# Optimization experiments

Measured on AMD Instinct MI355X. Metric: run time of the kernel, lower is better.

## Reference

```python
import jax, jax.numpy as jnp
import numpy as np

H, W = 2048, 4096
NUM_FRAMES, NUM_CAMERAS = 200, 4


def setup_inputs() -> dict:
    key = jax.random.key(0)
    k0, k1, k2, k3, k4 = jax.random.split(key, 5)
    exposure_params = 0.1 * jax.random.normal(k0, (NUM_FRAMES,), dtype=jnp.float32)
    vignetting_params = 0.05 * jax.random.normal(k1, (NUM_CAMERAS, 3, 5), dtype=jnp.float32)
    color_params = 0.05 * jax.random.normal(k2, (NUM_FRAMES, 8), dtype=jnp.float32)
    crf_params = 0.1 * jax.random.normal(k3, (NUM_CAMERAS, 3, 4), dtype=jnp.float32)
    rgb_in = jax.random.uniform(k4, (H, W, 3), dtype=jnp.float32)
    xs = jnp.arange(W, dtype=jnp.float32) + 0.5  # pixel-center x
    ys = jnp.arange(H, dtype=jnp.float32) + 0.5  # pixel-center y
    gx, gy = jnp.meshgrid(xs, ys)  # each [H, W]
    pixel_coords = jnp.stack([gx, gy], axis=-1)  # [H, W, 2] (x, y)
    return {
        'exposure_params': exposure_params,
        'vignetting_params': vignetting_params,
        'color_params': color_params,
        'crf_params': crf_params,
        'rgb_in': rgb_in,
        'pixel_coords': pixel_coords,
        'resolution_w': W,
        'resolution_h': H,
        'camera_idx': 1,
        'frame_idx': 3,
    }


def _ppisp_forward(exposure_params, vignetting_params, color_params, crf_params,
                   rgb_flat, coords_flat, resolution_w, resolution_h,
                   camera_idx, frame_idx):
    # rgb_flat: [N, 3], coords_flat: [N, 2]
    rgb = rgb_flat
    # --- stage 1: per-frame exposure scale ---
    if frame_idx >= 0:
        rgb = rgb * jnp.exp(exposure_params[frame_idx])
    # --- stage 2: per-camera radial vignetting polynomial (per channel) ---
    if camera_idx >= 0:
        vp = vignetting_params[camera_idx]  # [3, 5] = (cx, cy, a1, a2, a3) per channel
        cx = (0.5 + vp[:, 0]) * resolution_w   # [3] optical center x in pixels
        cy = (0.5 + vp[:, 1]) * resolution_h   # [3]
        norm2 = (0.5 * resolution_w) ** 2 + (0.5 * resolution_h) ** 2
        dx = coords_flat[:, :1] - cx           # [N, 3]
        dy = coords_flat[:, 1:] - cy           # [N, 3]
        r2 = (dx * dx + dy * dy) / norm2       # normalized squared radius
        vig = 1.0 + r2 * (vp[:, 2] + r2 * (vp[:, 3] + r2 * vp[:, 4]))  # Horner cubic in r^2
        rgb = rgb * vig
    # --- stage 3: per-frame 8-param color correction (identity-anchored 3x3) ---
    if frame_idx >= 0:
        p = color_params[frame_idx]  # [8]
        one = jnp.ones((), dtype=p.dtype)
        M = jnp.stack([
            jnp.stack([one + p[0], p[1], p[2]]),
            jnp.stack([p[3], one + p[4], p[5]]),
            jnp.stack([p[6], p[7], one]),
        ])  # [3, 3]
        rgb = rgb @ M.T
    # --- stage 4: per-camera CRF gamma curve (per channel, 4 params) ---
    if camera_idx >= 0:
        q = crf_params[camera_idx]      # [3, 4] = (log_gamma, b1, b2, b3)
        gamma = jnp.exp(q[:, 0])        # [3]
        x = jnp.clip(rgb, 0.0, 1.0)
        y = x ** gamma
        # smooth perturbation anchored at y=0 and y=1
        y = y + y * (1.0 - y) * (q[:, 1] + q[:, 2] * y + q[:, 3] * (1.0 - y))
        rgb = y
    return rgb


def reference(exposure_params, vignetting_params, color_params, crf_params,
              rgb_in, pixel_coords, resolution_w, resolution_h, camera_idx, frame_idx):
    original_shape = rgb_in.shape
    rgb_flat = rgb_in.reshape(-1, 3).astype(jnp.float32)
    coords_flat = pixel_coords.reshape(-1, 2).astype(jnp.float32)
    out = _ppisp_forward(exposure_params.astype(jnp.float32),
                         vignetting_params.astype(jnp.float32),
                         color_params.astype(jnp.float32),
                         crf_params.astype(jnp.float32),
                         rgb_flat, coords_flat,
                         int(resolution_w), int(resolution_h),
                         int(camera_idx), int(frame_idx))
    return out.reshape(original_shape)
```

## Files before the change

### kernel.cpp

```cpp
#include <hip/hip_runtime.h>
#include <math.h>

constexpr int W = 4096;
constexpr int H = 2048;
constexpr int W_SHIFT = 12;
constexpr int NPIX = W * H;
constexpr int NFLOAT = NPIX * 3;
constexpr int BLOCK = 256;
constexpr int WAVES = BLOCK / 64;
constexpr int PIX_PER_LANE = 4;
constexpr int FLT_PER_LANE = 3 * PIX_PER_LANE;
constexpr int CHUNK_FLT = 64 * FLT_PER_LANE;
constexpr int CHUNK_PIX = CHUNK_FLT / 3;
constexpr int GRID = NPIX / (WAVES * CHUNK_PIX);

#define AS1 __attribute__((address_space(1)))
#define AS3 __attribute__((address_space(3)))

__global__ __launch_bounds__(BLOCK) void ppisp_kernel(
    const float* __restrict__ exposure,
    const float* __restrict__ vigp,
    const float* __restrict__ colorp,
    const float* __restrict__ crfp,
    const float* __restrict__ rgb_in,
    const int*   __restrict__ cam_idx,
    const int*   __restrict__ frm_idx,
    float*       __restrict__ out)
{
    __shared__ float smem[WAVES][CHUNK_FLT];

    const int t    = threadIdx.x;
    const int wave = t >> 6;
    const int lane = t & 63;

    const int chunk = blockIdx.x * WAVES + wave;
    const size_t f0 = (size_t)chunk * CHUNK_FLT;

    #pragma unroll
    for (int j = 0; j < 3; ++j) {
        __builtin_amdgcn_global_load_lds(
            (const AS1 void*)(rgb_in + f0 + j * 256 + lane * 4),
            (AS3 void*)&smem[wave][j * 256], 16, 0, 0);
    }

    const int cam = cam_idx[0];
    const int frm = frm_idx[0];

    const float escale = (frm >= 0) ? __expf(exposure[frm]) : 1.0f;

    float cx[3], cy[3], a1[3], a2[3], a3[3];
    if (cam >= 0) {
        const float* vp = vigp + cam * 15;
        #pragma unroll
        for (int c = 0; c < 3; ++c) {
            cx[c] = (0.5f + vp[c * 5 + 0]) * (float)W;
            cy[c] = (0.5f + vp[c * 5 + 1]) * (float)H;
            a1[c] = vp[c * 5 + 2];
            a2[c] = vp[c * 5 + 3];
            a3[c] = vp[c * 5 + 4];
        }
    } else {
        #pragma unroll
        for (int c = 0; c < 3; ++c) {
            cx[c] = cy[c] = 0.0f;
            a1[c] = a2[c] = a3[c] = 0.0f;
        }
    }
    const float nx = 0.5f * (float)W, ny = 0.5f * (float)H;
    const float inv_norm2 = 1.0f / (nx * nx + ny * ny);

    float M[9];
    if (frm >= 0) {
        const float* p = colorp + frm * 8;
        M[0] = 1.0f + p[0]; M[1] = p[1];        M[2] = p[2];
        M[3] = p[3];        M[4] = 1.0f + p[4]; M[5] = p[5];
        M[6] = p[6];        M[7] = p[7];        M[8] = 1.0f;
    } else {
        M[0] = 1.0f; M[1] = 0.0f; M[2] = 0.0f;
        M[3] = 0.0f; M[4] = 1.0f; M[5] = 0.0f;
        M[6] = 0.0f; M[7] = 0.0f; M[8] = 1.0f;
    }

    float gam[3], b1[3], b2[3], b3[3];
    const int crf_on = (cam >= 0);
    if (crf_on) {
        const float* q = crfp + cam * 12;
        #pragma unroll
        for (int c = 0; c < 3; ++c) {
            gam[c] = __expf(q[c * 4 + 0]);
            b1[c]  = q[c * 4 + 1];
            b2[c]  = q[c * 4 + 2];
            b3[c]  = q[c * 4 + 3];
        }
    } else {
        #pragma unroll
        for (int c = 0; c < 3; ++c) { gam[c] = 1.0f; b1[c] = b2[c] = b3[c] = 0.0f; }
    }

    asm volatile("s_waitcnt vmcnt(0)" ::: "memory");
    __builtin_amdgcn_sched_barrier(0);

    const float4* sb = (const float4*)smem[wave];
    const float4 x0 = sb[lane * 3 + 0];
    const float4 x1 = sb[lane * 3 + 1];
    const float4 x2 = sb[lane * 3 + 2];

    float v[FLT_PER_LANE];
    v[0] = x0.x; v[1]  = x0.y; v[2]  = x0.z; v[3]  = x0.w;
    v[4] = x1.x; v[5]  = x1.y; v[6]  = x1.z; v[7]  = x1.w;
    v[8] = x2.x; v[9]  = x2.y; v[10] = x2.z; v[11] = x2.w;

    const int pb = chunk * CHUNK_PIX + lane * PIX_PER_LANE;
    #pragma unroll
    for (int k = 0; k < PIX_PER_LANE; ++k) {
        const int p = pb + k;
        const float px = (float)(p & (W - 1)) + 0.5f;
        const float py = (float)(p >> W_SHIFT) + 0.5f;

        float ch[3];
        #pragma unroll
        for (int c = 0; c < 3; ++c) ch[c] = v[k * 3 + c] * escale;

        #pragma unroll
        for (int c = 0; c < 3; ++c) {
            const float dx = px - cx[c];
            const float dy = py - cy[c];
            const float r2 = (dx * dx + dy * dy) * inv_norm2;
            ch[c] *= 1.0f + r2 * (a1[c] + r2 * (a2[c] + r2 * a3[c]));
        }

        float o[3];
        o[0] = M[0] * ch[0] + M[1] * ch[1] + M[2] * ch[2];
        o[1] = M[3] * ch[0] + M[4] * ch[1] + M[5] * ch[2];
        o[2] = M[6] * ch[0] + M[7] * ch[1] + M[8] * ch[2];

        if (crf_on) {
            #pragma unroll
            for (int c = 0; c < 3; ++c) {
                const float x = fminf(fmaxf(o[c], 0.0f), 1.0f);
                float y = exp2f(gam[c] * __log2f(x));
                y = y + y * (1.0f - y) * (b1[c] + b2[c] * y + b3[c] * (1.0f - y));
                o[c] = y;
            }
        }

        v[k * 3 + 0] = o[0];
        v[k * 3 + 1] = o[1];
        v[k * 3 + 2] = o[2];
    }

    float4* og = (float4*)(out + f0 + (size_t)lane * FLT_PER_LANE);
    og[0] = make_float4(v[0], v[1], v[2],  v[3]);
    og[1] = make_float4(v[4], v[5], v[6],  v[7]);
    og[2] = make_float4(v[8], v[9], v[10], v[11]);
}

extern "C" void kernel_launch(void* const* d_in, const int* in_sizes, int n_in,
                              void* d_out, int out_size, void* d_ws, size_t ws_size,
                              hipStream_t stream) {
    const float* exposure = (const float*)d_in[0];
    const float* vigp     = (const float*)d_in[1];
    const float* colorp   = (const float*)d_in[2];
    const float* crfp     = (const float*)d_in[3];
    const float* rgb_in   = (const float*)d_in[4];
    const int* cam_idx = (const int*)d_in[8];
    const int* frm_idx = (const int*)d_in[9];
    float* out = (float*)d_out;

    ppisp_kernel<<<dim3(GRID), dim3(BLOCK), 0, stream>>>(
        exposure, vigp, colorp, crfp, rgb_in, cam_idx, frm_idx, out);
}
```

Baseline: 228.2 us.

## Double pixels per lane and stage output through LDS with coalesced nontemporal stores

Each lane now handles 8 pixels in two halves of 4, loading 6 LDS-staged segments per wave and halving the grid. Results are written back into LDS and then stored to global memory in fully coalesced 16-byte-per-lane rows with nontemporal stores, replacing the old strided 48-byte-per-lane float4 writes. This targets write coalescing and cache pollution on a bandwidth-bound streaming kernel. It costs more LDS per block and fewer blocks in flight, which may reduce occupancy and latency hiding.

After: 222.2 us. 1.03x faster.

```diff
diff --git a/kernel.cpp b/kernel.cpp
--- a/kernel.cpp
+++ b/kernel.cpp
@@ -8,14 +8,16 @@
 constexpr int NFLOAT = NPIX * 3;
 constexpr int BLOCK = 256;
 constexpr int WAVES = BLOCK / 64;
-constexpr int PIX_PER_LANE = 4;
+constexpr int PIX_PER_LANE = 8;
 constexpr int FLT_PER_LANE = 3 * PIX_PER_LANE;
 constexpr int CHUNK_FLT = 64 * FLT_PER_LANE;
 constexpr int CHUNK_PIX = CHUNK_FLT / 3;
-constexpr int GRID = NPIX / (WAVES * CHUNK_PIX);
+constexpr int GRID = NFLOAT / (WAVES * CHUNK_FLT);
 
 #define AS1 __attribute__((address_space(1)))
 #define AS3 __attribute__((address_space(3)))
+
+typedef float floatx4 __attribute__((ext_vector_type(4)));
 
 __global__ __launch_bounds__(BLOCK) void ppisp_kernel(
     const float* __restrict__ exposure,
@@ -37,7 +39,7 @@
     const size_t f0 = (size_t)chunk * CHUNK_FLT;
 
     #pragma unroll
-    for (int j = 0; j < 3; ++j) {
+    for (int j = 0; j < 6; ++j) {
         __builtin_amdgcn_global_load_lds(
             (const AS1 void*)(rgb_in + f0 + j * 256 + lane * 4),
             (AS3 void*)&smem[wave][j * 256], 16, 0, 0);
@@ -100,59 +102,81 @@
     asm volatile("s_waitcnt vmcnt(0)" ::: "memory");
     __builtin_amdgcn_sched_barrier(0);
 
-    const float4* sb = (const float4*)smem[wave];
-    const float4 x0 = sb[lane * 3 + 0];
-    const float4 x1 = sb[lane * 3 + 1];
-    const float4 x2 = sb[lane * 3 + 2];
+    float4* sb = (float4*)smem[wave];
+    float v[FLT_PER_LANE];
+    #pragma unroll
+    for (int h = 0; h < 2; ++h) {
+        #pragma unroll
+        for (int j = 0; j < 3; ++j) {
+            const float4 x = sb[h * 192 + lane * 3 + j];
+            v[h * 12 + 4 * j + 0] = x.x;
+            v[h * 12 + 4 * j + 1] = x.y;
+            v[h * 12 + 4 * j + 2] = x.z;
+            v[h * 12 + 4 * j + 3] = x.w;
+        }
+    }
 
-    float v[FLT_PER_LANE];
-    v[0] = x0.x; v[1]  = x0.y; v[2]  = x0.z; v[3]  = x0.w;
-    v[4] = x1.x; v[5]  = x1.y; v[6]  = x1.z; v[7]  = x1.w;
-    v[8] = x2.x; v[9]  = x2.y; v[10] = x2.z; v[11] = x2.w;
+    #pragma unroll
+    for (int h = 0; h < 2; ++h) {
+        const int pb = chunk * CHUNK_PIX + h * 256 + lane * 4;
+        #pragma unroll
+        for (int k = 0; k < 4; ++k) {
+            const int p = pb + k;
+            const float px = (float)(p & (W - 1)) + 0.5f;
+            const float py = (float)(p >> W_SHIFT) + 0.5f;
 
-    const int pb = chunk * CHUNK_PIX + lane * PIX_PER_LANE;
-    #pragma unroll
-    for (int k = 0; k < PIX_PER_LANE; ++k) {
-        const int p = pb + k;
-        const float px = (float)(p & (W - 1)) + 0.5f;
-        const float py = (float)(p >> W_SHIFT) + 0.5f;
+            float ch[3];
+            #pragma unroll
+            for (int c = 0; c < 3; ++c) ch[c] = v[h * 12 + k * 3 + c] * escale;
 
-        float ch[3];
-        #pragma unroll
-        for (int c = 0; c < 3; ++c) ch[c] = v[k * 3 + c] * escale;
-
-        #pragma unroll
-        for (int c = 0; c < 3; ++c) {
-            const float dx = px - cx[c];
-            const float dy = py - cy[c];
-            const float r2 = (dx * dx + dy * dy) * inv_norm2;
-            ch[c] *= 1.0f + r2 * (a1[c] + r2 * (a2[c] + r2 * a3[c]));
-        }
-
-        float o[3];
-        o[0] = M[0] * ch[0] + M[1] * ch[1] + M[2] * ch[2];
-        o[1] = M[3] * ch[0] + M[4] * ch[1] + M[5] * ch[2];
-        o[2] = M[6] * ch[0] + M[7] * ch[1] + M[8] * ch[2];
-
-        if (crf_on) {
             #pragma unroll
             for (int c = 0; c < 3; ++c) {
-                const float x = fminf(fmaxf(o[c], 0.0f), 1.0f);
-                float y = exp2f(gam[c] * __log2f(x));
-                y = y + y * (1.0f - y) * (b1[c] + b2[c] * y + b3[c] * (1.0f - y));
-                o[c] = y;
+                const float dx = px - cx[c];
+                const float dy = py - cy[c];
+                const float r2 = (dx * dx + dy * dy) * inv_norm2;
+                ch[c] *= 1.0f + r2 * (a1[c] + r2 * (a2[c] + r2 * a3[c]));
             }
+
+            float o[3];
+            o[0] = M[0] * ch[0] + M[1] * ch[1] + M[2] * ch[2];
+            o[1] = M[3] * ch[0] + M[4] * ch[1] + M[5] * ch[2];
+            o[2] = M[6] * ch[0] + M[7] * ch[1] + M[8] * ch[2];
+
+            if (crf_on) {
+                #pragma unroll
+                for (int c = 0; c < 3; ++c) {
+                    const float x = fminf(fmaxf(o[c], 0.0f), 1.0f);
+                    float y = exp2f(gam[c] * __log2f(x));
+                    y = y + y * (1.0f - y) * (b1[c] + b2[c] * y + b3[c] * (1.0f - y));
+                    o[c] = y;
+                }
+            }
+
+            v[h * 12 + k * 3 + 0] = o[0];
+            v[h * 12 + k * 3 + 1] = o[1];
+            v[h * 12 + k * 3 + 2] = o[2];
         }
-
-        v[k * 3 + 0] = o[0];
-        v[k * 3 + 1] = o[1];
-        v[k * 3 + 2] = o[2];
     }
 
-    float4* og = (float4*)(out + f0 + (size_t)lane * FLT_PER_LANE);
-    og[0] = make_float4(v[0], v[1], v[2],  v[3]);
-    og[1] = make_float4(v[4], v[5], v[6],  v[7]);
-    og[2] = make_float4(v[8], v[9], v[10], v[11]);
+    #pragma unroll
+    for (int h = 0; h < 2; ++h) {
+        #pragma unroll
+        for (int j = 0; j < 3; ++j) {
+            sb[h * 192 + lane * 3 + j] =
+                make_float4(v[h * 12 + 4 * j + 0], v[h * 12 + 4 * j + 1],
+                            v[h * 12 + 4 * j + 2], v[h * 12 + 4 * j + 3]);
+        }
+    }
+
+    {
+        const floatx4* sl = (const floatx4*)smem[wave];
+        floatx4* og = (floatx4*)(out + f0);
+        #pragma unroll
+        for (int j = 0; j < 6; ++j) {
+            const floatx4 x = sl[j * 64 + lane];
+            __builtin_nontemporal_store(x, &og[j * 64 + lane]);
+        }
+    }
 }
 
 extern "C" void kernel_launch(void* const* d_in, const int* in_sizes, int n_in,
```

## Convert to persistent grid with 4-deep LDS prefetch pipeline and nontemporal coalesced stores

Applied to the files above, without the earlier changes.

Replaces the one-chunk-per-wave launch with a fixed grid of 768 blocks in which each wave loops over many chunks. Up to three future chunks are kept in flight through global_load_lds into a 4-slot per-wave LDS ring, with explicit vmcnt waits. Results are written back into LDS and then stored to global memory as fully coalesced nontemporal float4 stores instead of strided per-lane stores. This aims to hide load latency and improve write coalescing, but adds LDS traffic and makes correctness depend on hand-set vmcnt counts, and the final iterations clamp their prefetch to reload the last chunk.

After: 228.6 us. No clear change (+0.2%).

```diff
diff --git a/kernel.cpp b/kernel.cpp
--- a/kernel.cpp
+++ b/kernel.cpp
@@ -12,10 +12,16 @@
 constexpr int FLT_PER_LANE = 3 * PIX_PER_LANE;
 constexpr int CHUNK_FLT = 64 * FLT_PER_LANE;
 constexpr int CHUNK_PIX = CHUNK_FLT / 3;
-constexpr int GRID = NPIX / (WAVES * CHUNK_PIX);
+constexpr int NCHUNK = NFLOAT / CHUNK_FLT;
+constexpr int GRID = 768;
+constexpr int NWAVE = GRID * WAVES;
+constexpr int DEPTH = 4;
+constexpr int ITERS = (NCHUNK + NWAVE - 1) / NWAVE;
 
 #define AS1 __attribute__((address_space(1)))
 #define AS3 __attribute__((address_space(3)))
+
+typedef float floatx4 __attribute__((ext_vector_type(4)));
 
 __global__ __launch_bounds__(BLOCK) void ppisp_kernel(
     const float* __restrict__ exposure,
@@ -27,21 +33,12 @@
     const int*   __restrict__ frm_idx,
     float*       __restrict__ out)
 {
-    __shared__ float smem[WAVES][CHUNK_FLT];
+    __shared__ float smem[WAVES][DEPTH][CHUNK_FLT];
 
     const int t    = threadIdx.x;
     const int wave = t >> 6;
     const int lane = t & 63;
-
-    const int chunk = blockIdx.x * WAVES + wave;
-    const size_t f0 = (size_t)chunk * CHUNK_FLT;
-
-    #pragma unroll
-    for (int j = 0; j < 3; ++j) {
-        __builtin_amdgcn_global_load_lds(
-            (const AS1 void*)(rgb_in + f0 + j * 256 + lane * 4),
-            (AS3 void*)&smem[wave][j * 256], 16, 0, 0);
-    }
+    const int wgid = blockIdx.x * WAVES + wave;
 
     const int cam = cam_idx[0];
     const int frm = frm_idx[0];
@@ -98,61 +95,105 @@
     }
 
     asm volatile("s_waitcnt vmcnt(0)" ::: "memory");
-    __builtin_amdgcn_sched_barrier(0);
-
-    const float4* sb = (const float4*)smem[wave];
-    const float4 x0 = sb[lane * 3 + 0];
-    const float4 x1 = sb[lane * 3 + 1];
-    const float4 x2 = sb[lane * 3 + 2];
-
-    float v[FLT_PER_LANE];
-    v[0] = x0.x; v[1]  = x0.y; v[2]  = x0.z; v[3]  = x0.w;
-    v[4] = x1.x; v[5]  = x1.y; v[6]  = x1.z; v[7]  = x1.w;
-    v[8] = x2.x; v[9]  = x2.y; v[10] = x2.z; v[11] = x2.w;
-
-    const int pb = chunk * CHUNK_PIX + lane * PIX_PER_LANE;
+
     #pragma unroll
-    for (int k = 0; k < PIX_PER_LANE; ++k) {
-        const int p = pb + k;
-        const float px = (float)(p & (W - 1)) + 0.5f;
-        const float py = (float)(p >> W_SHIFT) + 0.5f;
-
-        float ch[3];
-        #pragma unroll
-        for (int c = 0; c < 3; ++c) ch[c] = v[k * 3 + c] * escale;
-
-        #pragma unroll
-        for (int c = 0; c < 3; ++c) {
-            const float dx = px - cx[c];
-            const float dy = py - cy[c];
-            const float r2 = (dx * dx + dy * dy) * inv_norm2;
-            ch[c] *= 1.0f + r2 * (a1[c] + r2 * (a2[c] + r2 * a3[c]));
-        }
-
-        float o[3];
-        o[0] = M[0] * ch[0] + M[1] * ch[1] + M[2] * ch[2];
-        o[1] = M[3] * ch[0] + M[4] * ch[1] + M[5] * ch[2];
-        o[2] = M[6] * ch[0] + M[7] * ch[1] + M[8] * ch[2];
-
-        if (crf_on) {
+    for (int d = 0; d < DEPTH - 1; ++d) {
+        const size_t f = (size_t)(wgid + d * NWAVE) * CHUNK_FLT;
+        #pragma unroll
+        for (int j = 0; j < 3; ++j) {
+            __builtin_amdgcn_global_load_lds(
+                (const AS1 void*)(rgb_in + f + j * 256 + lane * 4),
+                (AS3 void*)&smem[wave][d][j * 256], 16, 0, 0);
+        }
+    }
+
+    #pragma unroll
+    for (int i = 0; i < ITERS; ++i) {
+        {
+            int pcid = wgid + (i + DEPTH - 1) * NWAVE;
+            pcid = pcid < NCHUNK ? pcid : NCHUNK - 1;
+            const size_t f = (size_t)pcid * CHUNK_FLT;
             #pragma unroll
-            for (int c = 0; c < 3; ++c) {
-                const float x = fminf(fmaxf(o[c], 0.0f), 1.0f);
-                float y = exp2f(gam[c] * __log2f(x));
-                y = y + y * (1.0f - y) * (b1[c] + b2[c] * y + b3[c] * (1.0f - y));
-                o[c] = y;
+            for (int j = 0; j < 3; ++j) {
+                __builtin_amdgcn_global_load_lds(
+                    (const AS1 void*)(rgb_in + f + j * 256 + lane * 4),
+                    (AS3 void*)&smem[wave][(i + DEPTH - 1) & 3][j * 256],
+                    16, 0, 0);
             }
         }
 
-        v[k * 3 + 0] = o[0];
-        v[k * 3 + 1] = o[1];
-        v[k * 3 + 2] = o[2];
-    }
-
-    float4* og = (float4*)(out + f0 + (size_t)lane * FLT_PER_LANE);
-    og[0] = make_float4(v[0], v[1], v[2],  v[3]);
-    og[1] = make_float4(v[4], v[5], v[6],  v[7]);
-    og[2] = make_float4(v[8], v[9], v[10], v[11]);
+        if (i == 0)      asm volatile("s_waitcnt vmcnt(9)"  ::: "memory");
+        else if (i == 1) asm volatile("s_waitcnt vmcnt(12)" ::: "memory");
+        else if (i == 2) asm volatile("s_waitcnt vmcnt(15)" ::: "memory");
+        else             asm volatile("s_waitcnt vmcnt(18)" ::: "memory");
+        __builtin_amdgcn_sched_barrier(0);
+
+        const int cid = wgid + i * NWAVE;
+        if (cid < NCHUNK) {
+            float4* sb = (float4*)smem[wave][i & 3];
+            const float4 x0 = sb[lane * 3 + 0];
+            const float4 x1 = sb[lane * 3 + 1];
+            const float4 x2 = sb[lane * 3 + 2];
+
+            float v[FLT_PER_LANE];
+            v[0] = x0.x; v[1]  = x0.y; v[2]  = x0.z; v[3]  = x0.w;
+            v[4] = x1.x; v[5]  = x1.y; v[6]  = x1.z; v[7]  = x1.w;
+            v[8] = x2.x; v[9]  = x2.y; v[10] = x2.z; v[11] = x2.w;
+
+            const int pb = cid * CHUNK_PIX + lane * PIX_PER_LANE;
+            #pragma unroll
+            for (int k = 0; k < PIX_PER_LANE; ++k) {
+                const int p = pb + k;
+                const float px = (float)(p & (W - 1)) + 0.5f;
+                const float py = (float)(p >> W_SHIFT) + 0.5f;
+
+                float ch[3];
+                #pragma unroll
+                for (int c = 0; c < 3; ++c) ch[c] = v[k * 3 + c] * escale;
+
+                #pragma unroll
+                for (int c = 0; c < 3; ++c) {
+                    const float dx = px - cx[c];
+                    const float dy = py - cy[c];
+                    const float r2 = (dx * dx + dy * dy) * inv_norm2;
+                    ch[c] *= 1.0f + r2 * (a1[c] + r2 * (a2[c] + r2 * a3[c]));
+                }
+
+                float o[3];
+                o[0] = M[0] * ch[0] + M[1] * ch[1] + M[2] * ch[2];
+                o[1] = M[3] * ch[0] + M[4] * ch[1] + M[5] * ch[2];
+                o[2] = M[6] * ch[0] + M[7] * ch[1] + M[8] * ch[2];
+
+                if (crf_on) {
+                    #pragma unroll
+                    for (int c = 0; c < 3; ++c) {
+                        const float x = fminf(fmaxf(o[c], 0.0f), 1.0f);
+                        float y = exp2f(gam[c] * __log2f(x));
+                        y = y + y * (1.0f - y) * (b1[c] + b2[c] * y + b3[c] * (1.0f - y));
+                        o[c] = y;
+                    }
+                }
+
+                v[k * 3 + 0] = o[0];
+                v[k * 3 + 1] = o[1];
+                v[k * 3 + 2] = o[2];
+            }
+
+            sb[lane * 3 + 0] = make_float4(v[0], v[1], v[2],  v[3]);
+            sb[lane * 3 + 1] = make_float4(v[4], v[5], v[6],  v[7]);
+            sb[lane * 3 + 2] = make_float4(v[8], v[9], v[10], v[11]);
+
+            {
+                const floatx4* sl = (const floatx4*)smem[wave][i & 3];
+                floatx4* og = (floatx4*)(out + (size_t)cid * CHUNK_FLT);
+                #pragma unroll
+                for (int j = 0; j < 3; ++j) {
+                    const floatx4 x = sl[j * 64 + lane];
+                    __builtin_nontemporal_store(x, &og[j * 64 + lane]);
+                }
+            }
+        }
+    }
 }
 
 extern "C" void kernel_launch(void* const* d_in, const int* in_sizes, int n_in,
```
